# Performance work log

Hardware: AMD Instinct MI355X
Metric: run time of the kernel (lower is better)

The kernel has to match this reference:

```python
import jax, jax.numpy as jnp
import numpy as np

N, F_IN, F_OUT, K = 4096, 32, 32, 2
NEG_SLOPE = 0.2
MASK_VAL = -9e15


def _sparse_mat(kv, km, density=0.01):
    vals = jax.random.normal(kv, (N, N), dtype=jnp.float32)
    mask = jax.random.uniform(km, (N, N)) < density
    return vals * mask


def setup_inputs() -> dict:
    key = jax.random.key(0)
    ks = jax.random.split(key, 12)
    x = jax.random.normal(ks[0], (N, F_IN), dtype=jnp.float32)
    Ld = _sparse_mat(ks[1], ks[2])
    Lu = _sparse_mat(ks[3], ks[4])
    P = jax.random.normal(ks[5], (N, N), dtype=jnp.float32) / np.sqrt(N)
    W1 = jax.random.normal(ks[6], (K, F_IN, F_OUT), dtype=jnp.float32) * 0.1
    W2 = jax.random.normal(ks[7], (K, F_IN, F_OUT), dtype=jnp.float32) * 0.1
    W0 = jax.random.normal(ks[8], (F_IN, F_OUT), dtype=jnp.float32) * 0.1
    att1 = jax.random.normal(ks[9], (2 * F_OUT * K, 1), dtype=jnp.float32) * 0.1
    att2 = jax.random.normal(ks[10], (2 * F_OUT * K, 1), dtype=jnp.float32) * 0.1
    return {"x": x, "Ld": Ld, "Lu": Lu, "P": P, "W1": W1, "W2": W2,
            "W0": W0, "att1": att1, "att2": att2}


def _branch(x, L, W, att):
    # W: [K, F_in, F_out]; precompute x @ W[k] for all k -> [K, N, F_out]
    Kk, _, Fo = W.shape
    xw = jnp.einsum('nf,kfo->kno', x, W)
    # torch.cat([x@W[k]], dim=1) == transpose+reshape of xw
    xcat = jnp.transpose(xw, (1, 0, 2)).reshape(x.shape[0], Kk * Fo)
    d = Fo * Kk
    e = xcat @ att[:d] + (xcat @ att[d:]).T            # [N, N]
    e = jax.nn.leaky_relu(e, negative_slope=NEG_SLOPE)
    e = jnp.where(L != 0, e, MASK_VAL)
    alpha = jax.nn.softmax(e, axis=1)                   # row softmax, no dropout (eval)
    z = alpha @ xw[0]
    a = alpha
    for k in range(1, Kk):
        a = a @ L
        z = z + a @ xw[k]
    return z


def reference(x, Ld, Lu, P, W1, W2, W0, att1, att2):
    z1 = _branch(x, Ld, W1, att1)
    z2 = _branch(x, Lu, W2, att2)
    x0 = P @ (x @ W0)
    return z1 + z2 + x0
```

## Files before the change

### kernel.cpp

```cpp
#include <hip/hip_runtime.h>
#include <hip/hip_bf16.h>

#define NN 4096
#define CAP 128
#define KS 8
#define PGB 1024

typedef __attribute__((ext_vector_type(8))) short bf16x8;
typedef __attribute__((ext_vector_type(4))) float f32x4;

typedef __attribute__((address_space(1))) const void gas_t;
typedef __attribute__((address_space(3))) void las_t;
#define GLOAD_LDS16(gsrc, ldst) \
    __builtin_amdgcn_global_load_lds((gas_t*)(gsrc), (las_t*)(ldst), 16, 0, 0)

__device__ __forceinline__ float lrelu(float v) { return v >= 0.f ? v : 0.2f * v; }

__device__ __forceinline__ ushort f2bu(float f) {
    unsigned u = __float_as_uint(f);
    return (ushort)((u + 0x7FFFu + ((u >> 16) & 1u)) >> 16);
}

__global__ __launch_bounds__(256) void k_prep(
    const float* __restrict__ x,
    const float* __restrict__ W1, const float* __restrict__ W2,
    const float* __restrict__ W0,
    const float* __restrict__ att1, const float* __restrict__ att2,
    float* __restrict__ xwA1, float* __restrict__ xwB1,
    float* __restrict__ xwA2, float* __restrict__ xwB2,
    float* __restrict__ a1, float* __restrict__ b1,
    float* __restrict__ a2, float* __restrict__ b2,
    __hip_bfloat16* __restrict__ Bt)
{
    __shared__ float wl[5120];
    __shared__ float xs[256];
    const int t = threadIdx.x;
    for (int i = t; i < 2048; i += 256) { wl[i] = W1[i]; wl[2048 + i] = W2[i]; }
    for (int i = t; i < 1024; i += 256) wl[4096 + i] = W0[i];
    const int rowBase = blockIdx.x * 8;
    xs[t] = x[rowBase * 32 + t];
    __syncthreads();

    const int o = t & 31, r = t >> 5;
    const int row = rowBase + r;
    const float* xr = &xs[r * 32];
    float vA1 = 0.f, vB1 = 0.f, vA2 = 0.f, vB2 = 0.f, v0 = 0.f;
#pragma unroll
    for (int f = 0; f < 32; ++f) {
        const float xv = xr[f];
        vA1 += xv * wl[f * 32 + o];
        vB1 += xv * wl[1024 + f * 32 + o];
        vA2 += xv * wl[2048 + f * 32 + o];
        vB2 += xv * wl[3072 + f * 32 + o];
        v0  += xv * wl[4096 + f * 32 + o];
    }
    xwA1[row * 32 + o] = vA1;
    xwB1[row * 32 + o] = vB1;
    xwA2[row * 32 + o] = vA2;
    xwB2[row * 32 + o] = vB2;
    ((ushort*)Bt)[(size_t)o * NN + row] = f2bu(v0);

    float pa1 = vA1 * att1[o]      + vB1 * att1[32 + o];
    float pb1 = vA1 * att1[64 + o] + vB1 * att1[96 + o];
    float pa2 = vA2 * att2[o]      + vB2 * att2[32 + o];
    float pb2 = vA2 * att2[64 + o] + vB2 * att2[96 + o];
#pragma unroll
    for (int m = 1; m <= 16; m <<= 1) {
        pa1 += __shfl_xor(pa1, m); pb1 += __shfl_xor(pb1, m);
        pa2 += __shfl_xor(pa2, m); pb2 += __shfl_xor(pb2, m);
    }
    if (o == 0) { a1[row] = pa1; b1[row] = pb1; a2[row] = pa2; b2[row] = pb2; }
}

__global__ __launch_bounds__(128) void k_fused(
    const float* __restrict__ Ld, const float* __restrict__ Lu,
    const float* __restrict__ xwB1, const float* __restrict__ xwB2,
    const float* __restrict__ xwA1, const float* __restrict__ xwA2,
    const float* __restrict__ a1, const float* __restrict__ b1,
    const float* __restrict__ a2, const float* __restrict__ b2,
    int2* __restrict__ csrv, int* __restrict__ cntArr,
    float* __restrict__ u1, float* __restrict__ u2,
    const float* __restrict__ P, const ushort* __restrict__ Bt,
    float* __restrict__ partial)
{
    __shared__ float4 lrow[NN / 4];
    __shared__ int   sidx[CAP];
    __shared__ float sval[CAP];
    __shared__ float red[128];
    __shared__ float rpart[4];
    __shared__ int   lcnt;

    const int bid = blockIdx.x;
    const int t = threadIdx.x;
    const int lane = t & 63, w = t >> 6;

    if (bid < PGB) {
        const int gw = bid * 2 + w;
        const int mt = gw & 255;
        const int ks = gw >> 8;
        const int m0 = mt * 16;
        const int r  = lane & 15;
        const int kq = lane >> 4;

        const float*  pa  = P  + (size_t)(m0 + r) * NN + ks * 512 + kq * 8;
        const ushort* pb0 = Bt + (size_t)r        * NN + ks * 512 + kq * 8;
        const ushort* pb1 = Bt + (size_t)(16 + r) * NN + ks * 512 + kq * 8;

        f32x4 acc0 = {0.f, 0.f, 0.f, 0.f};
        f32x4 acc1 = {0.f, 0.f, 0.f, 0.f};

#pragma unroll 4
        for (int kk = 0; kk < 16; ++kk) {
            const float4 a0  = *(const float4*)(pa + kk * 32);
            const float4 a1v = *(const float4*)(pa + kk * 32 + 4);
            const bf16x8 b0  = *(const bf16x8*)(pb0 + kk * 32);
            const bf16x8 b1v = *(const bf16x8*)(pb1 + kk * 32);
            bf16x8 a;
            a[0] = (short)f2bu(a0.x);  a[1] = (short)f2bu(a0.y);
            a[2] = (short)f2bu(a0.z);  a[3] = (short)f2bu(a0.w);
            a[4] = (short)f2bu(a1v.x); a[5] = (short)f2bu(a1v.y);
            a[6] = (short)f2bu(a1v.z); a[7] = (short)f2bu(a1v.w);
            acc0 = __builtin_amdgcn_mfma_f32_16x16x32_bf16(a, b0, acc0, 0, 0, 0);
            acc1 = __builtin_amdgcn_mfma_f32_16x16x32_bf16(a, b1v, acc1, 0, 0, 0);
        }

        float* out = partial + ((size_t)ks * NN + m0 + kq * 4) * 32;
#pragma unroll
        for (int rr = 0; rr < 4; ++rr) {
            out[rr * 32 + r]      = acc0[rr];
            out[rr * 32 + 16 + r] = acc1[rr];
        }
        return;
    }

    const int sb  = bid - PGB;
    const int br  = sb >> 12;
    const int row = sb & (NN - 1);
    const float* L   = br ? Lu : Ld;
    const float* xwB = br ? xwB2 : xwB1;
    const float* xwA = br ? xwA2 : xwA1;
    const float* aA  = br ? a2 : a1;
    const float* bA  = br ? b2 : b1;
    int2* csrB = csrv + ((size_t)br * NN + row) * CAP;
    float* u   = br ? u2 : u1;

    if (t == 0) lcnt = 0;

    const float4* L4 = (const float4*)(L + (size_t)row * NN);
#pragma unroll
    for (int j = 0; j < 8; ++j) {
        GLOAD_LDS16(L4 + j * 128 + t, (char*)lrow + (j * 128 + w * 64) * 16);
    }
    asm volatile("s_waitcnt vmcnt(0)" ::: "memory");
    __syncthreads();

#pragma unroll
    for (int j = 0; j < 8; ++j) {
        const float4 v = lrow[j * 128 + t];
        const int c0 = (j * 128 + t) * 4;
        if (v.x != 0.f) { const int s = atomicAdd(&lcnt, 1); if (s < CAP) { sidx[s] = c0;     sval[s] = v.x; } }
        if (v.y != 0.f) { const int s = atomicAdd(&lcnt, 1); if (s < CAP) { sidx[s] = c0 + 1; sval[s] = v.y; } }
        if (v.z != 0.f) { const int s = atomicAdd(&lcnt, 1); if (s < CAP) { sidx[s] = c0 + 2; sval[s] = v.z; } }
        if (v.w != 0.f) { const int s = atomicAdd(&lcnt, 1); if (s < CAP) { sidx[s] = c0 + 3; sval[s] = v.w; } }
    }
    __syncthreads();

    const int cnt  = min(lcnt, CAP);
    const int cp32 = min((cnt + 31) & ~31, CAP);
    if (t >= cnt && t < cp32) { sidx[t] = 0; sval[t] = 0.f; }

    const float ai = aA[row];
    const int myidx = (t < cp32) ? sidx[t] : 0;
    const float e = (t < cnt) ? lrelu(ai + bA[myidx]) : -1e30f;
    float m = e;
#pragma unroll
    for (int mm = 1; mm <= 32; mm <<= 1) m = fmaxf(m, __shfl_xor(m, mm));
    if (lane == 0) rpart[w] = m;
    __syncthreads();
    m = fmaxf(rpart[0], rpart[1]);
    const float wgt = (t < cnt) ? __expf(e - m) : 0.f;
    float ss = wgt;
#pragma unroll
    for (int mm = 1; mm <= 32; mm <<= 1) ss += __shfl_xor(ss, mm);
    if (lane == 0) rpart[2 + w] = ss;
    __syncthreads();
    const float ssum = rpart[2] + rpart[3];
    const float inv = (cnt > 0) ? 1.f / ssum : 0.f;
    if (t < cp32) { int2 eo; eo.x = myidx; eo.y = __float_as_int(wgt * inv); csrB[t] = eo; }
    if (t == 0) cntArr[br * NN + row] = cnt;

    const int o = t & 31, g = t >> 5;
    float acc = 0.f;
    for (int s0 = 0; s0 < cp32; s0 += 32) {
        float vv[8], uu[8];
#pragma unroll
        for (int q = 0; q < 8; ++q) {
            const int sl = s0 + 4 * q + g;
            vv[q] = sval[sl];
            uu[q] = xwB[(size_t)sidx[sl] * 32 + o];
        }
#pragma unroll
        for (int q = 0; q < 8; ++q) acc += vv[q] * uu[q];
    }
    red[t] = acc;
    __syncthreads();
    if (t < 32) {
        const float tot2 = red[t] + red[32 + t] + red[64 + t] + red[96 + t];
        u[(size_t)row * 32 + t] = tot2 + xwA[(size_t)row * 32 + t];
    }
}

__global__ __launch_bounds__(256) void k_accum(
    const int2* __restrict__ csrv, const int* __restrict__ cntArr,
    const float* __restrict__ u1, const float* __restrict__ u2,
    const float* __restrict__ partial, float* __restrict__ outp)
{
    __shared__ int2 sle[4][2 * CAP];
    const int w = threadIdx.x >> 6, lane = threadIdx.x & 63;
    const int row = blockIdx.x * 4 + w;
    const int o = lane & 31, g = lane >> 5;
    int2* se = sle[w];

    float total = 0.f;
#pragma unroll
    for (int p = 0; p < KS; ++p)
        total += partial[(size_t)p * NN * 32 + (size_t)row * 32 + o];

    int cp[2];
#pragma unroll
    for (int br = 0; br < 2; ++br) {
        const int cnt = cntArr[br * NN + row];
        cp[br] = min((cnt + 31) & ~31, CAP);
        const int2* ci = csrv + ((size_t)br * NN + row) * CAP;
        if (lane < cp[br])      se[br * CAP + lane]      = ci[lane];
        if (lane + 64 < cp[br]) se[br * CAP + lane + 64] = ci[lane + 64];
    }

#pragma unroll
    for (int br = 0; br < 2; ++br) {
        const float* U = br ? u2 : u1;
        float acc = 0.f;
        const int nb = cp[br] >> 4;
        for (int j = 0; j < nb; ++j) {
            float wv[8], uv[8];
#pragma unroll
            for (int q = 0; q < 8; ++q) {
                const int2 e = se[br * CAP + 16 * j + 2 * q + g];
                wv[q] = __int_as_float(e.y);
                uv[q] = U[(size_t)e.x * 32 + o];
            }
#pragma unroll
            for (int q = 0; q < 8; ++q) acc += wv[q] * uv[q];
        }
        acc += __shfl_xor(acc, 32);
        total += acc;
    }

    if (lane < 32) outp[(size_t)row * 32 + o] = total;
}

extern "C" void kernel_launch(void* const* d_in, const int* in_sizes, int n_in,
                              void* d_out, int out_size, void* d_ws, size_t ws_size,
                              hipStream_t stream) {
    (void)in_sizes; (void)n_in; (void)out_size; (void)ws_size;
    const float* x    = (const float*)d_in[0];
    const float* Ld   = (const float*)d_in[1];
    const float* Lu   = (const float*)d_in[2];
    const float* P    = (const float*)d_in[3];
    const float* W1   = (const float*)d_in[4];
    const float* W2   = (const float*)d_in[5];
    const float* W0   = (const float*)d_in[6];
    const float* att1 = (const float*)d_in[7];
    const float* att2 = (const float*)d_in[8];

    float* ws = (float*)d_ws;
    float* xwA1 = ws;
    float* xwB1 = ws + 131072;
    float* xwA2 = ws + 262144;
    float* xwB2 = ws + 393216;
    float* u1   = ws + 524288;
    float* u2   = ws + 655360;
    float* a1   = ws + 786432;
    float* b1   = ws + 790528;
    float* a2   = ws + 794624;
    float* b2   = ws + 798720;
    float* partial = ws + 802816;
    __hip_bfloat16* Bt = (__hip_bfloat16*)(ws + 1851392);
    int2* csrv = (int2*)(ws + 1916928);
    int*  cnt  = (int*)(ws + 4014080);

    k_prep<<<512, 256, 0, stream>>>(x, W1, W2, W0, att1, att2,
                                    xwA1, xwB1, xwA2, xwB2, a1, b1, a2, b2, Bt);
    k_fused<<<PGB + 2 * NN, 128, 0, stream>>>(Ld, Lu, xwB1, xwB2, xwA1, xwA2,
                                              a1, b1, a2, b2, csrv, cnt, u1, u2,
                                              P, (const ushort*)Bt, partial);
    k_accum<<<NN / 4, 256, 0, stream>>>(csrv, cnt, u1, u2, partial,
                                        (float*)d_out);
}
```

Measured before the change: 220.9 us.

## Process eight L rows per block with double-buffered LDS prefetch

Measured after the change: 236.7 us. 1.07x slower.

```diff
diff --git a/kernel.cpp b/kernel.cpp
--- a/kernel.cpp
+++ b/kernel.cpp
@@ -4,6 +4,7 @@
 #define NN 4096
 #define CAP 128
 #define KS 8
+#define SCB 1024
 #define PGB 1024
 
 typedef __attribute__((ext_vector_type(8))) short bf16x8;
@@ -83,7 +84,7 @@
     const float* __restrict__ P, const ushort* __restrict__ Bt,
     float* __restrict__ partial)
 {
-    __shared__ float4 lrow[NN / 4];
+    __shared__ float4 lrow[2][NN / 4];
     __shared__ int   sidx[CAP];
     __shared__ float sval[CAP];
     __shared__ float red[128];
@@ -94,8 +95,8 @@
     const int t = threadIdx.x;
     const int lane = t & 63, w = t >> 6;
 
-    if (bid < PGB) {
-        const int gw = bid * 2 + w;
+    if (bid >= SCB) {
+        const int gw = (bid - SCB) * 2 + w;
         const int mt = gw & 255;
         const int ks = gw >> 8;
         const int m0 = mt * 16;
@@ -133,80 +134,97 @@
         return;
     }
 
-    const int sb  = bid - PGB;
-    const int br  = sb >> 12;
-    const int row = sb & (NN - 1);
-    const float* L   = br ? Lu : Ld;
-    const float* xwB = br ? xwB2 : xwB1;
-    const float* xwA = br ? xwA2 : xwA1;
-    const float* aA  = br ? a2 : a1;
-    const float* bA  = br ? b2 : b1;
-    int2* csrB = csrv + ((size_t)br * NN + row) * CAP;
-    float* u   = br ? u2 : u1;
-
-    if (t == 0) lcnt = 0;
-
-    const float4* L4 = (const float4*)(L + (size_t)row * NN);
-#pragma unroll
-    for (int j = 0; j < 8; ++j) {
-        GLOAD_LDS16(L4 + j * 128 + t, (char*)lrow + (j * 128 + w * 64) * 16);
-    }
-    asm volatile("s_waitcnt vmcnt(0)" ::: "memory");
-    __syncthreads();
-
-#pragma unroll
-    for (int j = 0; j < 8; ++j) {
-        const float4 v = lrow[j * 128 + t];
-        const int c0 = (j * 128 + t) * 4;
-        if (v.x != 0.f) { const int s = atomicAdd(&lcnt, 1); if (s < CAP) { sidx[s] = c0;     sval[s] = v.x; } }
-        if (v.y != 0.f) { const int s = atomicAdd(&lcnt, 1); if (s < CAP) { sidx[s] = c0 + 1; sval[s] = v.y; } }
-        if (v.z != 0.f) { const int s = atomicAdd(&lcnt, 1); if (s < CAP) { sidx[s] = c0 + 2; sval[s] = v.z; } }
-        if (v.w != 0.f) { const int s = atomicAdd(&lcnt, 1); if (s < CAP) { sidx[s] = c0 + 3; sval[s] = v.w; } }
-    }
-    __syncthreads();
-
-    const int cnt  = min(lcnt, CAP);
-    const int cp32 = min((cnt + 31) & ~31, CAP);
-    if (t >= cnt && t < cp32) { sidx[t] = 0; sval[t] = 0.f; }
-
-    const float ai = aA[row];
-    const int myidx = (t < cp32) ? sidx[t] : 0;
-    const float e = (t < cnt) ? lrelu(ai + bA[myidx]) : -1e30f;
-    float m = e;
-#pragma unroll
-    for (int mm = 1; mm <= 32; mm <<= 1) m = fmaxf(m, __shfl_xor(m, mm));
-    if (lane == 0) rpart[w] = m;
-    __syncthreads();
-    m = fmaxf(rpart[0], rpart[1]);
-    const float wgt = (t < cnt) ? __expf(e - m) : 0.f;
-    float ss = wgt;
-#pragma unroll
-    for (int mm = 1; mm <= 32; mm <<= 1) ss += __shfl_xor(ss, mm);
-    if (lane == 0) rpart[2 + w] = ss;
-    __syncthreads();
-    const float ssum = rpart[2] + rpart[3];
-    const float inv = (cnt > 0) ? 1.f / ssum : 0.f;
-    if (t < cp32) { int2 eo; eo.x = myidx; eo.y = __float_as_int(wgt * inv); csrB[t] = eo; }
-    if (t == 0) cntArr[br * NN + row] = cnt;
-
-    const int o = t & 31, g = t >> 5;
-    float acc = 0.f;
-    for (int s0 = 0; s0 < cp32; s0 += 32) {
-        float vv[8], uu[8];
-#pragma unroll
-        for (int q = 0; q < 8; ++q) {
-            const int sl = s0 + 4 * q + g;
-            vv[q] = sval[sl];
-            uu[q] = xwB[(size_t)sidx[sl] * 32 + o];
-        }
-#pragma unroll
-        for (int q = 0; q < 8; ++q) acc += vv[q] * uu[q];
-    }
-    red[t] = acc;
-    __syncthreads();
-    if (t < 32) {
-        const float tot2 = red[t] + red[32 + t] + red[64 + t] + red[96 + t];
-        u[(size_t)row * 32 + t] = tot2 + xwA[(size_t)row * 32 + t];
+    const int u0 = bid * 8;
+
+    {
+        const int br0 = u0 >> 12, row0 = u0 & (NN - 1);
+        const float4* L4 = (const float4*)((br0 ? Lu : Ld) + (size_t)row0 * NN);
+#pragma unroll
+        for (int j = 0; j < 8; ++j)
+            GLOAD_LDS16(L4 + j * 128 + t, (char*)lrow[0] + (j * 128 + w * 64) * 16);
+    }
+
+    for (int i = 0; i < 8; ++i) {
+        const int cur = i & 1;
+        const int uu = u0 + i;
+        const int br = uu >> 12, row = uu & (NN - 1);
+        const float* xwB = br ? xwB2 : xwB1;
+        const float* xwA = br ? xwA2 : xwA1;
+        const float* aA  = br ? a2 : a1;
+        const float* bA  = br ? b2 : b1;
+        int2* csrB = csrv + ((size_t)br * NN + row) * CAP;
+        float* u   = br ? u2 : u1;
+
+        if (t == 0) lcnt = 0;
+
+        if (i < 7) {
+            const int un = uu + 1;
+            const int brn = un >> 12, rown = un & (NN - 1);
+            const float4* Ln = (const float4*)((brn ? Lu : Ld) + (size_t)rown * NN);
+#pragma unroll
+            for (int j = 0; j < 8; ++j)
+                GLOAD_LDS16(Ln + j * 128 + t, (char*)lrow[cur ^ 1] + (j * 128 + w * 64) * 16);
+            asm volatile("s_waitcnt vmcnt(8)" ::: "memory");
+        } else {
+            asm volatile("s_waitcnt vmcnt(0)" ::: "memory");
+        }
+        __builtin_amdgcn_sched_barrier(0);
+        __syncthreads();
+
+#pragma unroll
+        for (int j = 0; j < 8; ++j) {
+            const float4 v = lrow[cur][j * 128 + t];
+            const int c0 = (j * 128 + t) * 4;
+            if (v.x != 0.f) { const int s = atomicAdd(&lcnt, 1); if (s < CAP) { sidx[s] = c0;     sval[s] = v.x; } }
+            if (v.y != 0.f) { const int s = atomicAdd(&lcnt, 1); if (s < CAP) { sidx[s] = c0 + 1; sval[s] = v.y; } }
+            if (v.z != 0.f) { const int s = atomicAdd(&lcnt, 1); if (s < CAP) { sidx[s] = c0 + 2; sval[s] = v.z; } }
+            if (v.w != 0.f) { const int s = atomicAdd(&lcnt, 1); if (s < CAP) { sidx[s] = c0 + 3; sval[s] = v.w; } }
+        }
+        __syncthreads();
+
+        const int cnt  = min(lcnt, CAP);
+        const int cp32 = min((cnt + 31) & ~31, CAP);
+        if (t >= cnt && t < cp32) { sidx[t] = 0; sval[t] = 0.f; }
+
+        const float ai = aA[row];
+        const int myidx = (t < cp32) ? sidx[t] : 0;
+        const float e = (t < cnt) ? lrelu(ai + bA[myidx]) : -1e30f;
+        float m = e;
+#pragma unroll
+        for (int mm = 1; mm <= 32; mm <<= 1) m = fmaxf(m, __shfl_xor(m, mm));
+        if (lane == 0) rpart[w] = m;
+        __syncthreads();
+        m = fmaxf(rpart[0], rpart[1]);
+        const float wgt = (t < cnt) ? __expf(e - m) : 0.f;
+        float ss = wgt;
+#pragma unroll
+        for (int mm = 1; mm <= 32; mm <<= 1) ss += __shfl_xor(ss, mm);
+        if (lane == 0) rpart[2 + w] = ss;
+        __syncthreads();
+        const float ssum = rpart[2] + rpart[3];
+        const float inv = (cnt > 0) ? 1.f / ssum : 0.f;
+        if (t < cp32) { int2 eo; eo.x = myidx; eo.y = __float_as_int(wgt * inv); csrB[t] = eo; }
+        if (t == 0) cntArr[br * NN + row] = cnt;
+
+        const int o = t & 31, g = t >> 5;
+        float acc = 0.f;
+        for (int s0 = 0; s0 < cp32; s0 += 32) {
+            float vv[8], uu2[8];
+#pragma unroll
+            for (int q = 0; q < 8; ++q) {
+                const int sl = s0 + 4 * q + g;
+                vv[q]  = sval[sl];
+                uu2[q] = xwB[(size_t)sidx[sl] * 32 + o];
+            }
+#pragma unroll
+            for (int q = 0; q < 8; ++q) acc += vv[q] * uu2[q];
+        }
+        red[t] = acc;
+        __syncthreads();
+        if (t < 32) {
+            const float tot2 = red[t] + red[32 + t] + red[64 + t] + red[96 + t];
+            u[(size_t)row * 32 + t] = tot2 + xwA[(size_t)row * 32 + t];
+        }
     }
 }
 
@@ -291,9 +309,9 @@
 
     k_prep<<<512, 256, 0, stream>>>(x, W1, W2, W0, att1, att2,
                                     xwA1, xwB1, xwA2, xwB2, a1, b1, a2, b2, Bt);
-    k_fused<<<PGB + 2 * NN, 128, 0, stream>>>(Ld, Lu, xwB1, xwB2, xwA1, xwA2,
-                                              a1, b1, a2, b2, csrv, cnt, u1, u2,
-                                              P, (const ushort*)Bt, partial);
+    k_fused<<<SCB + PGB, 128, 0, stream>>>(Ld, Lu, xwB1, xwB2, xwA1, xwA2,
+                                           a1, b1, a2, b2, csrv, cnt, u1, u2,
+                                           P, (const ushort*)Bt, partial);
     k_accum<<<NN / 4, 256, 0, stream>>>(csrv, cnt, u1, u2, partial,
                                         (float*)d_out);
 }
```
